# Optimization experiments

Hardware: AMD Instinct MI355X
Metric: run time of the kernel (lower is better)

Reference implementation:

```python
import jax, jax.numpy as jnp
import numpy as np

N, E = 50000, 800000
X_DIM, EA_DIM, H, L = 128, 16, 128, 3
BN_EPS = 1e-5


def setup_inputs() -> dict:
    key = jax.random.key(0)
    ks = jax.random.split(key, 20)
    s = 0.02
    inp = {
        "x": jax.random.normal(ks[0], (N, X_DIM), jnp.float32),
        "edge_index": jax.random.randint(ks[1], (2, E), 0, N, jnp.int64),
        "batch": jnp.sort(jax.random.randint(ks[2], (N,), 0, 128, jnp.int64)),
        "edge_attr": jax.random.normal(ks[3], (E, EA_DIM), jnp.float32),
        "edge_atten": jax.random.uniform(ks[4], (E, 1), jnp.float32),
        # node_encoder2 and edge_encoder
        "W_enc": jax.random.normal(ks[5], (X_DIM, H), jnp.float32) * s,
        "b_enc": jnp.zeros((H,), jnp.float32),
        "W_ee": jax.random.normal(ks[6], (EA_DIM, H), jnp.float32) * s,
        "b_ee": jnp.zeros((H,), jnp.float32),
        # per-layer GINEConv params (stacked over layers)
        "eps": jnp.zeros((L,), jnp.float32),
        "W1": jax.random.normal(ks[7], (L, H, H), jnp.float32) * s,
        "b1": jnp.zeros((L, H), jnp.float32),
        "bn_gamma": jnp.ones((L, H), jnp.float32),
        "bn_beta": jnp.zeros((L, H), jnp.float32),
        "bn_mean": jnp.zeros((L, H), jnp.float32),
        "bn_var": jnp.ones((L, H), jnp.float32),
        "W2": jax.random.normal(ks[8], (L, H, H), jnp.float32) * s,
        "b2": jnp.zeros((L, H), jnp.float32),
    }
    return inp


def reference(x, edge_index, batch, edge_attr, edge_atten,
              W_enc, b_enc, W_ee, b_ee, eps,
              W1, b1, bn_gamma, bn_beta, bn_mean, bn_var, W2, b2):
    # node/edge encoders
    h = x @ W_enc + b_enc                      # [N, H]
    ea = edge_attr @ W_ee + b_ee               # [E, H]
    src, dst = edge_index[0], edge_index[1]
    n = h.shape[0]
    for i in range(L):
        # GINEConv message: relu(x_j + edge_attr) * edge_atten, scatter-add to dst
        m = jax.nn.relu(h[src] + ea) * edge_atten          # [E, H]
        aggr = jax.ops.segment_sum(m, dst, num_segments=n) # [N, H]
        z = (1.0 + eps[i]) * h + aggr
        # MLP: Linear -> BatchNorm(eval, running stats) -> ReLU -> Linear
        z = z @ W1[i] + b1[i]
        z = (z - bn_mean[i]) * jax.lax.rsqrt(bn_var[i] + BN_EPS) * bn_gamma[i] + bn_beta[i]
        z = jax.nn.relu(z)
        z = z @ W2[i] + b2[i]
        # outer relu; dropout is identity in eval mode
        h = jax.nn.relu(z)
    return h
```

## Files before the change

kernel.cpp:

```cpp
#include <hip/hip_runtime.h>
#include <hip/hip_fp16.h>
#include <cstdint>
#include <cstddef>


typedef _Float16 f16x8 __attribute__((ext_vector_type(8)));
typedef float    f32x4 __attribute__((ext_vector_type(4)));

template <class T>
__device__ inline auto add2_impl(T* p, T v, int)
    -> decltype(unsafeAtomicAdd(p, v), void()) {
    unsafeAtomicAdd(p, v);
}
template <class T>
__device__ inline void add2_impl(T* p, T v, long) {
    unsafeAtomicAdd(&p->x, v.x);
    unsafeAtomicAdd(&p->y, v.y);
}
__device__ inline void atomic_add2(float* p, float x, float y) {
    add2_impl(reinterpret_cast<float2*>(p), make_float2(x, y), 0);
}

__global__ void zero_cnt(int* __restrict__ cnt, int N)
{
    int i = blockIdx.x * blockDim.x + threadIdx.x;
    if (i < N) cnt[i] = 0;
}

__global__ void fill_neg1(int* __restrict__ a, int n)
{
    int i = blockIdx.x * blockDim.x + threadIdx.x;
    const int st = gridDim.x * blockDim.x;
    for (; i < n; i += st) a[i] = -1;
}

__global__ void hist_kernel(const int* __restrict__ ei, int* __restrict__ cnt, int E)
{
    int i = blockIdx.x * blockDim.x + threadIdx.x;
    const int st = gridDim.x * blockDim.x;
    for (; i < E; i += st) atomicAdd(&cnt[ei[E + i]], 1);
}

__global__ __launch_bounds__(256) void scan_pass1(
    const int* __restrict__ cnt, int* __restrict__ bsum, int N)
{
    __shared__ int part[256];
    const int t = threadIdx.x;
    const int base = blockIdx.x * 1024 + t * 4;
    int s = 0;
#pragma unroll
    for (int j = 0; j < 4; ++j) {
        int idx = base + j;
        if (idx < N) { int v = cnt[idx]; s += v + (v & 1); }
    }
    part[t] = s;
    __syncthreads();
    for (int d = 128; d > 0; d >>= 1) {
        if (t < d) part[t] += part[t + d];
        __syncthreads();
    }
    if (t == 0) bsum[blockIdx.x] = part[0];
}

__global__ __launch_bounds__(256) void scan_pass2(
    int* __restrict__ bsum, int* __restrict__ off, int NB, int N)
{
    __shared__ int sb[1024];
    const int t = threadIdx.x;
    for (int i = t; i < NB; i += 256) sb[i] = bsum[i];
    __syncthreads();
    if (t == 0) {
        int run = 0;
        for (int i = 0; i < NB; ++i) { int v = sb[i]; sb[i] = run; run += v; }
        off[N] = run;
    }
    __syncthreads();
    for (int i = t; i < NB; i += 256) bsum[i] = sb[i];
}

__global__ __launch_bounds__(256) void scan_pass3(
    const int* __restrict__ cnt, const int* __restrict__ bsum,
    int* __restrict__ off, int* __restrict__ cur, int N)
{
    __shared__ int part[256];
    const int t = threadIdx.x;
    const int base = blockIdx.x * 1024 + t * 4;
    int pv[4]; int s = 0;
#pragma unroll
    for (int j = 0; j < 4; ++j) {
        int idx = base + j;
        int v = (idx < N) ? cnt[idx] : 0;
        pv[j] = v + (v & 1);
        s += pv[j];
    }
    part[t] = s;
    __syncthreads();
    for (int d = 1; d < 256; d <<= 1) {
        int x = (t >= d) ? part[t - d] : 0;
        __syncthreads();
        part[t] += x;
        __syncthreads();
    }
    int run = bsum[blockIdx.x] + part[t] - s;
#pragma unroll
    for (int j = 0; j < 4; ++j) {
        int idx = base + j;
        if (idx < N) { off[idx] = run; cur[idx] = run; }
        run += pv[j];
    }
}

__global__ void scatter_kernel(const int* __restrict__ ei, int* __restrict__ cur,
                               int* __restrict__ eids, int E)
{
    int i = blockIdx.x * blockDim.x + threadIdx.x;
    const int st = gridDim.x * blockDim.x;
    for (; i < E; i += st) {
        int pos = atomicAdd(&cur[ei[E + i]], 1);
        eids[pos] = i;
    }
}

__global__ void permute_sat(
    const int* __restrict__ ei, const float* __restrict__ eatten,
    const int* __restrict__ eids, const int* __restrict__ offN,
    float2* __restrict__ sat, int Scap)
{
    const int S = *offN;
    int i = blockIdx.x * blockDim.x + threadIdx.x;
    const int st = gridDim.x * blockDim.x;
    for (; i < Scap; i += st) {
        if (i >= S) break;
        const int eid = eids[i];
        float2 v;
        if (eid >= 0) { v.x = __int_as_float(ei[eid]); v.y = eatten[eid]; }
        else          { v.x = __int_as_float(0);       v.y = 0.f; }
        sat[i] = v;
    }
}

__global__ __launch_bounds__(256) void eabuild_staged(
    const int* __restrict__ eids, const float* __restrict__ eattr,
    const float* __restrict__ W_ee, const float* __restrict__ b_ee,
    const int* __restrict__ offN, uint32_t* __restrict__ eab2, int Scap)
{
    __shared__ int   se[256];
    __shared__ float sattr[256 * 16];
    const int t = threadIdx.x;
    const int lane = t & 63;
    const int wv = t >> 6;
    const int c = lane * 2;

    const int S = *offN;
    const int base = blockIdx.x * 256;
    const int n = min(256, S - base);
    if (n <= 0) return;

    float2 w[16];
#pragma unroll
    for (int k = 0; k < 16; ++k) w[k] = *(const float2*)&W_ee[k * 128 + c];
    const float2 bv = *(const float2*)&b_ee[c];

    if (t < n) se[t] = eids[base + t];
    __syncthreads();

    float4* sa4 = (float4*)sattr;
    const float4* ea4 = (const float4*)eattr;
    for (int i = t; i < n * 4; i += 256) {
        const int row = i >> 2, part = i & 3;
        const int eid = se[row];
        sa4[i] = (eid >= 0) ? ea4[(size_t)eid * 4 + part]
                            : make_float4(0.f, 0.f, 0.f, 0.f);
    }
    __syncthreads();

    for (int slot = wv; slot < n; slot += 4) {
        const int gs = base + slot;
        uint32_t out = 0;
        if (se[slot] >= 0) {
            const float4* sr = (const float4*)&sattr[slot * 16];
            float4 e0 = sr[0], e1 = sr[1], e2 = sr[2], e3 = sr[3];
            const float ef[16] = {e0.x, e0.y, e0.z, e0.w, e1.x, e1.y, e1.z, e1.w,
                                  e2.x, e2.y, e2.z, e2.w, e3.x, e3.y, e3.z, e3.w};
            float d0 = bv.x, d1 = bv.y;
#pragma unroll
            for (int k = 0; k < 16; ++k) {
                d0 = fmaf(ef[k], w[k].x, d0);
                d1 = fmaf(ef[k], w[k].y, d1);
            }
            __half2 hh = __floats2half2_rn(d0, d1);
            out = *reinterpret_cast<uint32_t*>(&hh);
        }
        eab2[(size_t)(gs >> 1) * 128 + lane * 2 + (gs & 1)] = out;
    }
}

__global__ void prepack_w(const float* __restrict__ W1, const float* __restrict__ W2,
                          const float* __restrict__ Wenc,
                          _Float16* __restrict__ Wpk, int L)
{
    int tid = blockIdx.x * blockDim.x + threadIdx.x;
    const int total = (2 * L + 1) * 32 * 64;
    if (tid >= total) return;
    const int lane = tid & 63;
    const int f = (tid >> 6) & 31;
    const int lm = tid >> 11;
    const int kb = f >> 3, tc = f & 7;
    const float* src = (lm < L) ? (W1 + (size_t)lm * 16384)
                    : (lm < 2 * L) ? (W2 + (size_t)(lm - L) * 16384)
                    : Wenc;
    _Float16* dst = Wpk + ((size_t)lm * 32 + f) * 512 + lane * 8;
#pragma unroll
    for (int i = 0; i < 8; ++i) {
        const int k = kb * 32 + (lane >> 4) * 8 + i;
        const int col = tc * 16 + (lane & 15);
        dst[i] = (_Float16)src[k * 128 + col];
    }
}

__global__ void cvt_f16(const float* __restrict__ x, _Float16* __restrict__ y, int n8)
{
    int i = blockIdx.x * blockDim.x + threadIdx.x;
    const int st = gridDim.x * blockDim.x;
    for (; i < n8; i += st) {
        float4 a = ((const float4*)x)[2 * i];
        float4 b = ((const float4*)x)[2 * i + 1];
        f16x8 v = {(_Float16)a.x, (_Float16)a.y, (_Float16)a.z, (_Float16)a.w,
                   (_Float16)b.x, (_Float16)b.y, (_Float16)b.z, (_Float16)b.w};
        ((f16x8*)y)[i] = v;
    }
}

__global__ __launch_bounds__(256) void enc_mfma(
    const _Float16* __restrict__ x16, const _Float16* __restrict__ Wpk,
    const float* __restrict__ bias, _Float16* __restrict__ h16, int n)
{
    const int t = threadIdx.x;
    const int lane = t & 63;
    const int w = t >> 6;
    const int row0 = blockIdx.x * 64;
    const int lr = lane & 15;
    const int lg = lane >> 4;

    f32x4 acc[8];
#pragma unroll
    for (int tc = 0; tc < 8; ++tc) acc[tc] = (f32x4){0.f, 0.f, 0.f, 0.f};
    const int arow = min(row0 + w * 16 + lr, n - 1);
#pragma unroll
    for (int kb = 0; kb < 4; ++kb) {
        f16x8 a = *(const f16x8*)&x16[(size_t)arow * 128 + kb * 32 + lg * 8];
#pragma unroll
        for (int tc = 0; tc < 8; ++tc) {
            f16x8 b = *(const f16x8*)&Wpk[((kb * 8 + tc) * 64 + lane) * 8];
            acc[tc] = __builtin_amdgcn_mfma_f32_16x16x32_f16(a, b, acc[tc], 0, 0, 0);
        }
    }
#pragma unroll
    for (int tc = 0; tc < 8; ++tc) {
        const int col = tc * 16 + lr;
        const float bb = bias[col];
#pragma unroll
        for (int j = 0; j < 4; ++j) {
            const int row = row0 + w * 16 + lg * 4 + j;
            if (row < n)
                h16[(size_t)row * 128 + col] = (_Float16)(acc[tc][j] + bb);
        }
    }
}

__global__ __launch_bounds__(256) void agg_f16(
    const _Float16* __restrict__ h16, const float2* __restrict__ sat,
    const uint32_t* __restrict__ eab2, const int* __restrict__ off,
    _Float16* __restrict__ z16, const float* __restrict__ eps, int layer, int N)
{
    const int t = threadIdx.x;
    const int v = blockIdx.x * 4 + (t >> 6);
    if (v >= N) return;
    const int lane = t & 63;
    const int c = lane * 2;

    const int e0 = off[v], e1 = off[v + 1];
    float a0 = 0.f, a1 = 0.f;
    int e = e0;
    for (; e + 8 <= e1; e += 8) {
        float4 sa[4];
#pragma unroll
        for (int j = 0; j < 4; ++j) sa[j] = *(const float4*)&sat[e + 2 * j];
        uint2 eb[4];
#pragma unroll
        for (int j = 0; j < 4; ++j)
            eb[j] = *(const uint2*)&eab2[(size_t)((e >> 1) + j) * 128 + lane * 2];
        uint32_t hv[8];
#pragma unroll
        for (int j = 0; j < 4; ++j) {
            hv[2 * j]     = *(const uint32_t*)&h16[(size_t)__float_as_int(sa[j].x) * 128 + c];
            hv[2 * j + 1] = *(const uint32_t*)&h16[(size_t)__float_as_int(sa[j].z) * 128 + c];
        }
#pragma unroll
        for (int j = 0; j < 4; ++j) {
            __half2 hh0 = *reinterpret_cast<const __half2*>(&hv[2 * j]);
            __half2 q0 = *reinterpret_cast<const __half2*>(&eb[j].x);
            a0 += fmaxf(__half2float(__low2half(hh0)) + __half2float(__low2half(q0)), 0.f) * sa[j].y;
            a1 += fmaxf(__half2float(__high2half(hh0)) + __half2float(__high2half(q0)), 0.f) * sa[j].y;
            __half2 hh1 = *reinterpret_cast<const __half2*>(&hv[2 * j + 1]);
            __half2 q1 = *reinterpret_cast<const __half2*>(&eb[j].y);
            a0 += fmaxf(__half2float(__low2half(hh1)) + __half2float(__low2half(q1)), 0.f) * sa[j].w;
            a1 += fmaxf(__half2float(__high2half(hh1)) + __half2float(__high2half(q1)), 0.f) * sa[j].w;
        }
    }
    for (; e < e1; e += 2) {
        float4 sa = *(const float4*)&sat[e];
        uint2 eb = *(const uint2*)&eab2[(size_t)(e >> 1) * 128 + lane * 2];
        uint32_t h0 = *(const uint32_t*)&h16[(size_t)__float_as_int(sa.x) * 128 + c];
        uint32_t h1 = *(const uint32_t*)&h16[(size_t)__float_as_int(sa.z) * 128 + c];
        __half2 hh0 = *reinterpret_cast<const __half2*>(&h0);
        __half2 q0 = *reinterpret_cast<const __half2*>(&eb.x);
        a0 += fmaxf(__half2float(__low2half(hh0)) + __half2float(__low2half(q0)), 0.f) * sa.y;
        a1 += fmaxf(__half2float(__high2half(hh0)) + __half2float(__high2half(q0)), 0.f) * sa.y;
        __half2 hh1 = *reinterpret_cast<const __half2*>(&h1);
        __half2 q1 = *reinterpret_cast<const __half2*>(&eb.y);
        a0 += fmaxf(__half2float(__low2half(hh1)) + __half2float(__low2half(q1)), 0.f) * sa.w;
        a1 += fmaxf(__half2float(__high2half(hh1)) + __half2float(__high2half(q1)), 0.f) * sa.w;
    }

    const float sc = 1.0f + eps[layer];
    uint32_t hv = *(const uint32_t*)&h16[(size_t)v * 128 + c];
    __half2 hh = *reinterpret_cast<const __half2*>(&hv);
    float zx = fmaf(sc, __half2float(__low2half(hh)), a0);
    float zy = fmaf(sc, __half2float(__high2half(hh)), a1);
    __half2 zz = __floats2half2_rn(zx, zy);
    *reinterpret_cast<__half2*>(&z16[(size_t)v * 128 + c]) = zz;
}

__global__ __launch_bounds__(256) void mlp_mfma(
    const _Float16* __restrict__ z16,
    const _Float16* __restrict__ W1pk, const float* __restrict__ b1,
    const float* __restrict__ gam, const float* __restrict__ bet,
    const float* __restrict__ mu, const float* __restrict__ var,
    const _Float16* __restrict__ W2pk, const float* __restrict__ b2,
    _Float16* __restrict__ h16out, float* __restrict__ H, int last, int n)
{
    __shared__ _Float16 Yt[64][136];
    const int t = threadIdx.x;
    const int lane = t & 63;
    const int w = t >> 6;
    const int row0 = blockIdx.x * 64;
    const int lr = lane & 15;
    const int lg = lane >> 4;

    f32x4 acc[8];
#pragma unroll
    for (int tc = 0; tc < 8; ++tc) acc[tc] = (f32x4){0.f, 0.f, 0.f, 0.f};
    const int arow = min(row0 + w * 16 + lr, n - 1);
#pragma unroll
    for (int kb = 0; kb < 4; ++kb) {
        f16x8 a = *(const f16x8*)&z16[(size_t)arow * 128 + kb * 32 + lg * 8];
#pragma unroll
        for (int tc = 0; tc < 8; ++tc) {
            f16x8 b = *(const f16x8*)&W1pk[((kb * 8 + tc) * 64 + lane) * 8];
            acc[tc] = __builtin_amdgcn_mfma_f32_16x16x32_f16(a, b, acc[tc], 0, 0, 0);
        }
    }
#pragma unroll
    for (int tc = 0; tc < 8; ++tc) {
        const int col = tc * 16 + lr;
        const float s  = gam[col] * rsqrtf(var[col] + 1e-5f);
        const float sh = bet[col] - mu[col] * s;
        const float bb = b1[col];
#pragma unroll
        for (int j = 0; j < 4; ++j) {
            float y = fmaxf(fmaf(acc[tc][j] + bb, s, sh), 0.f);
            Yt[w * 16 + lg * 4 + j][col] = (_Float16)y;
        }
    }
    __syncthreads();

#pragma unroll
    for (int tc = 0; tc < 8; ++tc) acc[tc] = (f32x4){0.f, 0.f, 0.f, 0.f};
#pragma unroll
    for (int kb = 0; kb < 4; ++kb) {
        f16x8 a = *(const f16x8*)&Yt[w * 16 + lr][kb * 32 + lg * 8];
#pragma unroll
        for (int tc = 0; tc < 8; ++tc) {
            f16x8 b = *(const f16x8*)&W2pk[((kb * 8 + tc) * 64 + lane) * 8];
            acc[tc] = __builtin_amdgcn_mfma_f32_16x16x32_f16(a, b, acc[tc], 0, 0, 0);
        }
    }
#pragma unroll
    for (int tc = 0; tc < 8; ++tc) {
        const int col = tc * 16 + lr;
        const float bb = b2[col];
#pragma unroll
        for (int j = 0; j < 4; ++j) {
            const int row = row0 + w * 16 + lg * 4 + j;
            if (row < n) {
                const float o = fmaxf(acc[tc][j] + bb, 0.f);
                if (last) H[(size_t)row * 128 + col] = o;
                else      h16out[(size_t)row * 128 + col] = (_Float16)o;
            }
        }
    }
}

__global__ __launch_bounds__(512, 4) void gemm_enc(
    const float* __restrict__ A, const float* __restrict__ W,
    const float* __restrict__ bias, float* __restrict__ H, int n)
{
    __shared__ float At[64][128];
    __shared__ float Wb[2][16][128];
    const int t = threadIdx.x;
    const int tx = t & 31, ty = t >> 5;

    const int row0 = blockIdx.x * 64;
    const int nrows = min(64, n - row0);
    const int lim = nrows * 32;
    const float4* A4 = (const float4*)(A + (size_t)row0 * 128);
    float4* At4 = (float4*)&At[0][0];
#pragma unroll
    for (int i = 0; i < 4; ++i) {
        int idx = t + 512 * i;
        if (idx < lim) At4[idx] = A4[idx];
    }
    const float4* W4 = (const float4*)W;
    ((float4*)&Wb[0][0][0])[t] = W4[t];
    __syncthreads();

    float acc[4][4] = {};
    for (int c = 0; c < 8; ++c) {
        const int buf = c & 1;
        float4 wnext;
        if (c < 7) wnext = W4[(c + 1) * 512 + t];
#pragma unroll
        for (int g = 0; g < 4; ++g) {
            float4 w4[4];
#pragma unroll
            for (int kk = 0; kk < 4; ++kk) w4[kk] = *(const float4*)&Wb[buf][g * 4 + kk][tx * 4];
#pragma unroll
            for (int r = 0; r < 4; ++r) {
                float4 a = *(const float4*)&At[ty * 4 + r][c * 16 + g * 4];
                float ar[4] = {a.x, a.y, a.z, a.w};
#pragma unroll
                for (int kk = 0; kk < 4; ++kk) {
                    acc[r][0] = fmaf(ar[kk], w4[kk].x, acc[r][0]);
                    acc[r][1] = fmaf(ar[kk], w4[kk].y, acc[r][1]);
                    acc[r][2] = fmaf(ar[kk], w4[kk].z, acc[r][2]);
                    acc[r][3] = fmaf(ar[kk], w4[kk].w, acc[r][3]);
                }
            }
        }
        if (c < 7) ((float4*)&Wb[buf ^ 1][0][0])[t] = wnext;
        __syncthreads();
    }

    const int c0 = tx * 4;
    float bvv[4];
#pragma unroll
    for (int c = 0; c < 4; ++c) bvv[c] = bias[c0 + c];
#pragma unroll
    for (int r = 0; r < 4; ++r) {
        int row = row0 + ty * 4 + r;
        if (row < n) {
            float4 o;
            o.x = acc[r][0] + bvv[0]; o.y = acc[r][1] + bvv[1];
            o.z = acc[r][2] + bvv[2]; o.w = acc[r][3] + bvv[3];
            *(float4*)&H[(size_t)row * 128 + c0] = o;
        }
    }
}

__global__ void scale_init(const float* __restrict__ h, float* __restrict__ z,
                           const float* __restrict__ eps, int layer, int n4)
{
    const float s = 1.0f + eps[layer];
    int i = blockIdx.x * blockDim.x + threadIdx.x;
    const int stride = gridDim.x * blockDim.x;
    const float4* h4 = (const float4*)h;
    float4* z4 = (float4*)z;
    for (; i < n4; i += stride) {
        float4 v = h4[i];
        v.x *= s; v.y *= s; v.z *= s; v.w *= s;
        z4[i] = v;
    }
}

__global__ __launch_bounds__(256) void edge_atomic(
    const float* __restrict__ h, const int* __restrict__ ei,
    const float* __restrict__ eattr, const float* __restrict__ eatten,
    const float* __restrict__ W_ee, const float* __restrict__ b_ee,
    float* __restrict__ Z, int E)
{
    __shared__ float Wee[16][128];
    __shared__ float bee[128];
    const int t = threadIdx.x;
    const float4* We4 = (const float4*)W_ee;
    float4* Ws4 = (float4*)&Wee[0][0];
#pragma unroll
    for (int i = 0; i < 2; ++i) Ws4[t + 256 * i] = We4[t + 256 * i];
    if (t < 128) bee[t] = b_ee[t];
    __syncthreads();

    const int lane = t & 63;
    const int c = lane * 2;
    const long wid = (long)blockIdx.x * 4 + (t >> 6);
    const long nw = (long)gridDim.x * 4;
    for (long e = wid; e < E; e += nw) {
        const int src = ei[e];
        const int dst = ei[E + e];
        const float att = eatten[e];
        union { float4 v4[4]; float f[16]; } ea;
        const float4* eap = (const float4*)(eattr + e * 16);
        ea.v4[0] = eap[0]; ea.v4[1] = eap[1]; ea.v4[2] = eap[2]; ea.v4[3] = eap[3];
        float2 hv = *(const float2*)&h[(size_t)src * 128 + c];
        float e0 = bee[c], e1 = bee[c + 1];
#pragma unroll
        for (int k = 0; k < 16; ++k) {
            float2 w = *(const float2*)&Wee[k][c];
            e0 = fmaf(ea.f[k], w.x, e0);
            e1 = fmaf(ea.f[k], w.y, e1);
        }
        float m0 = fmaxf(hv.x + e0, 0.f) * att;
        float m1 = fmaxf(hv.y + e1, 0.f) * att;
        atomic_add2(&Z[(size_t)dst * 128 + c], m0, m1);
    }
}

__global__ __launch_bounds__(512, 4) void gemm_mlp(
    const float* __restrict__ Z,
    const float* __restrict__ W1, const float* __restrict__ b1,
    const float* __restrict__ gam, const float* __restrict__ bet,
    const float* __restrict__ mu, const float* __restrict__ var,
    const float* __restrict__ W2, const float* __restrict__ b2,
    float* __restrict__ H, int n)
{
    __shared__ float At[64][128];
    __shared__ float Wb[2][16][128];
    const int t = threadIdx.x;
    const int tx = t & 31, ty = t >> 5;

    const int row0 = blockIdx.x * 64;
    const int nrows = min(64, n - row0);
    const int lim = nrows * 32;
    const float4* Z4 = (const float4*)(Z + (size_t)row0 * 128);
    float4* At4 = (float4*)&At[0][0];
#pragma unroll
    for (int i = 0; i < 4; ++i) {
        int idx = t + 512 * i;
        if (idx < lim) At4[idx] = Z4[idx];
    }
    const float4* W14 = (const float4*)W1;
    ((float4*)&Wb[0][0][0])[t] = W14[t];
    __syncthreads();

    float acc[4][4] = {};
    for (int c = 0; c < 8; ++c) {
        const int buf = c & 1;
        float4 wnext;
        if (c < 7) wnext = W14[(c + 1) * 512 + t];
#pragma unroll
        for (int g = 0; g < 4; ++g) {
            float4 w4[4];
#pragma unroll
            for (int kk = 0; kk < 4; ++kk) w4[kk] = *(const float4*)&Wb[buf][g * 4 + kk][tx * 4];
#pragma unroll
            for (int r = 0; r < 4; ++r) {
                float4 a = *(const float4*)&At[ty * 4 + r][c * 16 + g * 4];
                float ar[4] = {a.x, a.y, a.z, a.w};
#pragma unroll
                for (int kk = 0; kk < 4; ++kk) {
                    acc[r][0] = fmaf(ar[kk], w4[kk].x, acc[r][0]);
                    acc[r][1] = fmaf(ar[kk], w4[kk].y, acc[r][1]);
                    acc[r][2] = fmaf(ar[kk], w4[kk].z, acc[r][2]);
                    acc[r][3] = fmaf(ar[kk], w4[kk].w, acc[r][3]);
                }
            }
        }
        if (c < 7) ((float4*)&Wb[buf ^ 1][0][0])[t] = wnext;
        __syncthreads();
    }

    const int c0 = tx * 4;
    const float4* W24 = (const float4*)W2;
    float4 w2pre = W24[t];
    {
        float b1v[4], scv[4], shv[4];
#pragma unroll
        for (int cl = 0; cl < 4; ++cl) {
            b1v[cl] = b1[c0 + cl];
            float s = gam[c0 + cl] * rsqrtf(var[c0 + cl] + 1e-5f);
            scv[cl] = s;
            shv[cl] = bet[c0 + cl] - mu[c0 + cl] * s;
        }
#pragma unroll
        for (int r = 0; r < 4; ++r) {
            float4 y;
            y.x = fmaxf(fmaf(acc[r][0] + b1v[0], scv[0], shv[0]), 0.f);
            y.y = fmaxf(fmaf(acc[r][1] + b1v[1], scv[1], shv[1]), 0.f);
            y.z = fmaxf(fmaf(acc[r][2] + b1v[2], scv[2], shv[2]), 0.f);
            y.w = fmaxf(fmaf(acc[r][3] + b1v[3], scv[3], shv[3]), 0.f);
            *(float4*)&At[ty * 4 + r][c0] = y;
            acc[r][0] = 0.f; acc[r][1] = 0.f; acc[r][2] = 0.f; acc[r][3] = 0.f;
        }
    }
    ((float4*)&Wb[0][0][0])[t] = w2pre;
    __syncthreads();

    for (int c = 0; c < 8; ++c) {
        const int buf = c & 1;
        float4 wnext;
        if (c < 7) wnext = W24[(c + 1) * 512 + t];
#pragma unroll
        for (int g = 0; g < 4; ++g) {
            float4 w4[4];
#pragma unroll
            for (int kk = 0; kk < 4; ++kk) w4[kk] = *(const float4*)&Wb[buf][g * 4 + kk][tx * 4];
#pragma unroll
            for (int r = 0; r < 4; ++r) {
                float4 a = *(const float4*)&At[ty * 4 + r][c * 16 + g * 4];
                float ar[4] = {a.x, a.y, a.z, a.w};
#pragma unroll
                for (int kk = 0; kk < 4; ++kk) {
                    acc[r][0] = fmaf(ar[kk], w4[kk].x, acc[r][0]);
                    acc[r][1] = fmaf(ar[kk], w4[kk].y, acc[r][1]);
                    acc[r][2] = fmaf(ar[kk], w4[kk].z, acc[r][2]);
                    acc[r][3] = fmaf(ar[kk], w4[kk].w, acc[r][3]);
                }
            }
        }
        if (c < 7) ((float4*)&Wb[buf ^ 1][0][0])[t] = wnext;
        __syncthreads();
    }

    float b2v[4];
#pragma unroll
    for (int cl = 0; cl < 4; ++cl) b2v[cl] = b2[c0 + cl];
#pragma unroll
    for (int r = 0; r < 4; ++r) {
        int row = row0 + ty * 4 + r;
        if (row < n) {
            float4 o;
            o.x = fmaxf(acc[r][0] + b2v[0], 0.f);
            o.y = fmaxf(acc[r][1] + b2v[1], 0.f);
            o.z = fmaxf(acc[r][2] + b2v[2], 0.f);
            o.w = fmaxf(acc[r][3] + b2v[3], 0.f);
            *(float4*)&H[(size_t)row * 128 + c0] = o;
        }
    }
}

extern "C" void kernel_launch(void* const* d_in, const int* in_sizes, int n_in,
                              void* d_out, int out_size, void* d_ws, size_t ws_size,
                              hipStream_t stream)
{
    const float* x      = (const float*)d_in[0];
    const int*   ei     = (const int*)d_in[1];
    const float* eattr  = (const float*)d_in[3];
    const float* eatten = (const float*)d_in[4];
    const float* W_enc  = (const float*)d_in[5];
    const float* b_enc  = (const float*)d_in[6];
    const float* W_ee   = (const float*)d_in[7];
    const float* b_ee   = (const float*)d_in[8];
    const float* eps    = (const float*)d_in[9];
    const float* W1     = (const float*)d_in[10];
    const float* b1     = (const float*)d_in[11];
    const float* gam    = (const float*)d_in[12];
    const float* bet    = (const float*)d_in[13];
    const float* mu     = (const float*)d_in[14];
    const float* var    = (const float*)d_in[15];
    const float* W2     = (const float*)d_in[16];
    const float* b2     = (const float*)d_in[17];

    const int N = in_sizes[0] / 128;
    const int E = in_sizes[1] / 2;
    const int L = in_sizes[9];
    const int Scap = E + N;

    float* hout = (float*)d_out;

    char* p = (char*)d_ws;
    _Float16* z16 = (_Float16*)p;       p += ((size_t)N * 128 * 2 + 255) & ~(size_t)255;
    _Float16* h16 = (_Float16*)p;       p += ((size_t)N * 128 * 2 + 255) & ~(size_t)255;
    int* off  = (int*)p;                p += 4 * (size_t)(N + 1);
    int* cur  = (int*)p;                p += 4 * (size_t)N;
    int* cnt  = (int*)p;                p += 4 * (size_t)N;
    int* bsum = (int*)p;                p += 4 * 1024;
    int* eids = (int*)p;                p += 4 * (size_t)Scap;
    p = (char*)(((uintptr_t)p + 255) & ~(uintptr_t)255);
    float2* sat = (float2*)p;           p += 8 * (size_t)Scap;
    p = (char*)(((uintptr_t)p + 255) & ~(uintptr_t)255);
    uint32_t* eab2 = (uint32_t*)p;      p += 512 * (size_t)((Scap + 1) / 2);
    p = (char*)(((uintptr_t)p + 255) & ~(uintptr_t)255);
    _Float16* Wpk = (_Float16*)p;       p += (2 * (size_t)L + 1) * 32 * 512 * 2;
    const size_t need_main = (size_t)(p - (char*)d_ws);

    const bool use_main = ws_size >= need_main;
    const int tiles = (N + 63) / 64;
    const int NB = (N + 1023) / 1024;

    if (use_main) {
        _Float16* x16 = z16;

        zero_cnt<<<(N + 255) / 256, 256, 0, stream>>>(cnt, N);
        hist_kernel<<<1024, 256, 0, stream>>>(ei, cnt, E);
        scan_pass1<<<NB, 256, 0, stream>>>(cnt, bsum, N);
        scan_pass2<<<1, 256, 0, stream>>>(bsum, off, NB, N);
        scan_pass3<<<NB, 256, 0, stream>>>(cnt, bsum, off, cur, N);
        fill_neg1<<<1024, 256, 0, stream>>>(eids, Scap);
        scatter_kernel<<<1024, 256, 0, stream>>>(ei, cur, eids, E);
        permute_sat<<<1024, 256, 0, stream>>>(ei, eatten, eids, off + N, sat, Scap);
        eabuild_staged<<<(Scap + 255) / 256, 256, 0, stream>>>(
            eids, eattr, W_ee, b_ee, off + N, eab2, Scap);
        prepack_w<<<((2 * L + 1) * 32 * 64 + 255) / 256, 256, 0, stream>>>(
            W1, W2, W_enc, Wpk, L);

        cvt_f16<<<2048, 256, 0, stream>>>(x, x16, N * 128 / 8);
        enc_mfma<<<tiles, 256, 0, stream>>>(
            x16, Wpk + (size_t)(2 * L) * 32 * 512, b_enc, h16, N);

        for (int i = 0; i < L; ++i) {
            agg_f16<<<(N + 3) / 4, 256, 0, stream>>>(
                h16, sat, eab2, off, z16, eps, i, N);
            mlp_mfma<<<tiles, 256, 0, stream>>>(
                z16,
                Wpk + (size_t)i * 32 * 512, b1 + i * 128,
                gam + i * 128, bet + i * 128, mu + i * 128, var + i * 128,
                Wpk + (size_t)(L + i) * 32 * 512, b2 + i * 128,
                h16, hout, (i == L - 1) ? 1 : 0, N);
        }
        return;
    }

    float* zbuf = (float*)d_ws;
    float* h = hout;
    gemm_enc<<<tiles, 512, 0, stream>>>(x, W_enc, b_enc, h, N);
    for (int i = 0; i < L; ++i) {
        scale_init<<<2048, 256, 0, stream>>>(h, zbuf, eps, i, N * 128 / 4);
        edge_atomic<<<2048, 256, 0, stream>>>(h, ei, eattr, eatten, W_ee, b_ee, zbuf, E);
        gemm_mlp<<<tiles, 512, 0, stream>>>(
            zbuf, W1 + (size_t)i * 128 * 128, b1 + i * 128,
            gam + i * 128, bet + i * 128, mu + i * 128, var + i * 128,
            W2 + (size_t)i * 128 * 128, b2 + i * 128,
            h, N);
    }
}
```

Baseline: 480.8 us.

## Recompute edge encoder per edge in aggregation instead of materializing edge embeddings

```diff
diff --git a/kernel.cpp b/kernel.cpp
--- a/kernel.cpp
+++ b/kernel.cpp
@@ -5,7 +5,16 @@
 
 
 typedef _Float16 f16x8 __attribute__((ext_vector_type(8)));
+typedef _Float16 f16x2 __attribute__((ext_vector_type(2)));
 typedef float    f32x4 __attribute__((ext_vector_type(4)));
+
+__device__ inline float fdot2f(f16x2 a, f16x2 b, float c) {
+#if __has_builtin(__builtin_amdgcn_fdot2)
+    return __builtin_amdgcn_fdot2(a, b, c, false);
+#else
+    return c + (float)a.x * (float)b.x + (float)a.y * (float)b.y;
+#endif
+}
 
 template <class T>
 __device__ inline auto add2_impl(T* p, T v, int)
@@ -121,77 +130,33 @@
     }
 }
 
-__global__ void permute_sat(
+__global__ void permute_all(
     const int* __restrict__ ei, const float* __restrict__ eatten,
-    const int* __restrict__ eids, const int* __restrict__ offN,
-    float2* __restrict__ sat, int Scap)
+    const float* __restrict__ eattr, const int* __restrict__ eids,
+    const int* __restrict__ offN,
+    float2* __restrict__ sat, _Float16* __restrict__ attr16, int Scap)
 {
     const int S = *offN;
     int i = blockIdx.x * blockDim.x + threadIdx.x;
     const int st = gridDim.x * blockDim.x;
-    for (; i < Scap; i += st) {
-        if (i >= S) break;
+    for (; i < S; i += st) {
         const int eid = eids[i];
         float2 v;
-        if (eid >= 0) { v.x = __int_as_float(ei[eid]); v.y = eatten[eid]; }
-        else          { v.x = __int_as_float(0);       v.y = 0.f; }
+        f16x8 a0 = {}, a1 = {};
+        if (eid >= 0) {
+            v.x = __int_as_float(ei[eid]); v.y = eatten[eid];
+            const float4* ep = (const float4*)(eattr + (size_t)eid * 16);
+            float4 e0 = ep[0], e1 = ep[1], e2 = ep[2], e3 = ep[3];
+            a0 = (f16x8){(_Float16)e0.x, (_Float16)e0.y, (_Float16)e0.z, (_Float16)e0.w,
+                         (_Float16)e1.x, (_Float16)e1.y, (_Float16)e1.z, (_Float16)e1.w};
+            a1 = (f16x8){(_Float16)e2.x, (_Float16)e2.y, (_Float16)e2.z, (_Float16)e2.w,
+                         (_Float16)e3.x, (_Float16)e3.y, (_Float16)e3.z, (_Float16)e3.w};
+        } else {
+            v.x = __int_as_float(0); v.y = 0.f;
+        }
         sat[i] = v;
-    }
-}
-
-__global__ __launch_bounds__(256) void eabuild_staged(
-    const int* __restrict__ eids, const float* __restrict__ eattr,
-    const float* __restrict__ W_ee, const float* __restrict__ b_ee,
-    const int* __restrict__ offN, uint32_t* __restrict__ eab2, int Scap)
-{
-    __shared__ int   se[256];
-    __shared__ float sattr[256 * 16];
-    const int t = threadIdx.x;
-    const int lane = t & 63;
-    const int wv = t >> 6;
-    const int c = lane * 2;
-
-    const int S = *offN;
-    const int base = blockIdx.x * 256;
-    const int n = min(256, S - base);
-    if (n <= 0) return;
-
-    float2 w[16];
-#pragma unroll
-    for (int k = 0; k < 16; ++k) w[k] = *(const float2*)&W_ee[k * 128 + c];
-    const float2 bv = *(const float2*)&b_ee[c];
-
-    if (t < n) se[t] = eids[base + t];
-    __syncthreads();
-
-    float4* sa4 = (float4*)sattr;
-    const float4* ea4 = (const float4*)eattr;
-    for (int i = t; i < n * 4; i += 256) {
-        const int row = i >> 2, part = i & 3;
-        const int eid = se[row];
-        sa4[i] = (eid >= 0) ? ea4[(size_t)eid * 4 + part]
-                            : make_float4(0.f, 0.f, 0.f, 0.f);
-    }
-    __syncthreads();
-
-    for (int slot = wv; slot < n; slot += 4) {
-        const int gs = base + slot;
-        uint32_t out = 0;
-        if (se[slot] >= 0) {
-            const float4* sr = (const float4*)&sattr[slot * 16];
-            float4 e0 = sr[0], e1 = sr[1], e2 = sr[2], e3 = sr[3];
-            const float ef[16] = {e0.x, e0.y, e0.z, e0.w, e1.x, e1.y, e1.z, e1.w,
-                                  e2.x, e2.y, e2.z, e2.w, e3.x, e3.y, e3.z, e3.w};
-            float d0 = bv.x, d1 = bv.y;
-#pragma unroll
-            for (int k = 0; k < 16; ++k) {
-                d0 = fmaf(ef[k], w[k].x, d0);
-                d1 = fmaf(ef[k], w[k].y, d1);
-            }
-            __half2 hh = __floats2half2_rn(d0, d1);
-            out = *reinterpret_cast<uint32_t*>(&hh);
-        }
-        eab2[(size_t)(gs >> 1) * 128 + lane * 2 + (gs & 1)] = out;
+        ((f16x8*)attr16)[2 * i]     = a0;
+        ((f16x8*)attr16)[2 * i + 1] = a1;
     }
 }
 
@@ -270,62 +235,84 @@
 
 __global__ __launch_bounds__(256) void agg_f16(
     const _Float16* __restrict__ h16, const float2* __restrict__ sat,
-    const uint32_t* __restrict__ eab2, const int* __restrict__ off,
+    const _Float16* __restrict__ attr16, const int* __restrict__ off,
+    const float* __restrict__ W_ee, const float* __restrict__ b_ee,
     _Float16* __restrict__ z16, const float* __restrict__ eps, int layer, int N)
 {
     const int t = threadIdx.x;
+    const int lane = t & 63;
+    const int c = lane * 2;
+
+    f16x2 wx[8], wy[8];
+#pragma unroll
+    for (int j = 0; j < 8; ++j) {
+        float2 wa = *(const float2*)&W_ee[(2 * j) * 128 + c];
+        float2 wb = *(const float2*)&W_ee[(2 * j + 1) * 128 + c];
+        wx[j] = (f16x2){(_Float16)wa.x, (_Float16)wb.x};
+        wy[j] = (f16x2){(_Float16)wa.y, (_Float16)wb.y};
+    }
+    const float2 bv = *(const float2*)&b_ee[c];
+
     const int v = blockIdx.x * 4 + (t >> 6);
     if (v >= N) return;
-    const int lane = t & 63;
-    const int c = lane * 2;
 
     const int e0 = off[v], e1 = off[v + 1];
     float a0 = 0.f, a1 = 0.f;
+
+    auto edge = [&](uint4 lo, uint4 hi, uint32_t hvv, float att) {
+        const f16x2* a2lo = (const f16x2*)&lo;
+        const f16x2* a2hi = (const f16x2*)&hi;
+        float d0 = bv.x, d1 = bv.y;
+#pragma unroll
+        for (int j = 0; j < 4; ++j) {
+            d0 = fdot2f(a2lo[j], wx[j], d0);
+            d1 = fdot2f(a2lo[j], wy[j], d1);
+        }
+#pragma unroll
+        for (int j = 0; j < 4; ++j) {
+            d0 = fdot2f(a2hi[j], wx[4 + j], d0);
+            d1 = fdot2f(a2hi[j], wy[4 + j], d1);
+        }
+        __half2 hh = *reinterpret_cast<const __half2*>(&hvv);
+        a0 += fmaxf(__half2float(__low2half(hh)) + d0, 0.f) * att;
+        a1 += fmaxf(__half2float(__high2half(hh)) + d1, 0.f) * att;
+    };
+
     int e = e0;
-    for (; e + 8 <= e1; e += 8) {
-        float4 sa[4];
-#pragma unroll
-        for (int j = 0; j < 4; ++j) sa[j] = *(const float4*)&sat[e + 2 * j];
-        uint2 eb[4];
-#pragma unroll
-        for (int j = 0; j < 4; ++j)
-            eb[j] = *(const uint2*)&eab2[(size_t)((e >> 1) + j) * 128 + lane * 2];
-        uint32_t hv[8];
-#pragma unroll
-        for (int j = 0; j < 4; ++j) {
-            hv[2 * j]     = *(const uint32_t*)&h16[(size_t)__float_as_int(sa[j].x) * 128 + c];
-            hv[2 * j + 1] = *(const uint32_t*)&h16[(size_t)__float_as_int(sa[j].z) * 128 + c];
-        }
-#pragma unroll
-        for (int j = 0; j < 4; ++j) {
-            __half2 hh0 = *reinterpret_cast<const __half2*>(&hv[2 * j]);
-            __half2 q0 = *reinterpret_cast<const __half2*>(&eb[j].x);
-            a0 += fmaxf(__half2float(__low2half(hh0)) + __half2float(__low2half(q0)), 0.f) * sa[j].y;
-            a1 += fmaxf(__half2float(__high2half(hh0)) + __half2float(__high2half(q0)), 0.f) * sa[j].y;
-            __half2 hh1 = *reinterpret_cast<const __half2*>(&hv[2 * j + 1]);
-            __half2 q1 = *reinterpret_cast<const __half2*>(&eb[j].y);
-            a0 += fmaxf(__half2float(__low2half(hh1)) + __half2float(__low2half(q1)), 0.f) * sa[j].w;
-            a1 += fmaxf(__half2float(__high2half(hh1)) + __half2float(__high2half(q1)), 0.f) * sa[j].w;
-        }
+    for (; e + 4 <= e1; e += 4) {
+        float4 sa0 = *(const float4*)&sat[e];
+        float4 sa1 = *(const float4*)&sat[e + 2];
+        uint4 at[8];
+#pragma unroll
+        for (int u = 0; u < 4; ++u) {
+            at[2 * u]     = *(const uint4*)&attr16[(size_t)(e + u) * 16];
+            at[2 * u + 1] = *(const uint4*)&attr16[(size_t)(e + u) * 16 + 8];
+        }
+        uint32_t hv[4];
+        hv[0] = *(const uint32_t*)&h16[(size_t)__float_as_int(sa0.x) * 128 + c];
+        hv[1] = *(const uint32_t*)&h16[(size_t)__float_as_int(sa0.z) * 128 + c];
+        hv[2] = *(const uint32_t*)&h16[(size_t)__float_as_int(sa1.x) * 128 + c];
+        hv[3] = *(const uint32_t*)&h16[(size_t)__float_as_int(sa1.z) * 128 + c];
+        edge(at[0], at[1], hv[0], sa0.y);
+        edge(at[2], at[3], hv[1], sa0.w);
+        edge(at[4], at[5], hv[2], sa1.y);
+        edge(at[6], at[7], hv[3], sa1.w);
     }
     for (; e < e1; e += 2) {
         float4 sa = *(const float4*)&sat[e];
-        uint2 eb = *(const uint2*)&eab2[(size_t)(e >> 1) * 128 + lane * 2];
-        uint32_t h0 = *(const uint32_t*)&h16[(size_t)__float_as_int(sa.x) * 128 + c];
-        uint32_t h1 = *(const uint32_t*)&h16[(size_t)__float_as_int(sa.z) * 128 + c];
-        __half2 hh0 = *reinterpret_cast<const __half2*>(&h0);
-        __half2 q0 = *reinterpret_cast<const __half2*>(&eb.x);
-        a0 += fmaxf(__half2float(__low2half(hh0)) + __half2float(__low2half(q0)), 0.f) * sa.y;
-        a1 += fmaxf(__half2float(__high2half(hh0)) + __half2float(__high2half(q0)), 0.f) * sa.y;
-        __half2 hh1 = *reinterpret_cast<const __half2*>(&h1);
-        __half2 q1 = *reinterpret_cast<const __half2*>(&eb.y);
-        a0 += fmaxf(__half2float(__low2half(hh1)) + __half2float(__low2half(q1)), 0.f) * sa.w;
-        a1 += fmaxf(__half2float(__high2half(hh1)) + __half2float(__high2half(q1)), 0.f) * sa.w;
+        uint4 l0 = *(const uint4*)&attr16[(size_t)e * 16];
+        uint4 h0 = *(const uint4*)&attr16[(size_t)e * 16 + 8];
+        uint4 l1 = *(const uint4*)&attr16[(size_t)(e + 1) * 16];
+        uint4 h1 = *(const uint4*)&attr16[(size_t)(e + 1) * 16 + 8];
+        uint32_t hv0 = *(const uint32_t*)&h16[(size_t)__float_as_int(sa.x) * 128 + c];
+        uint32_t hv1 = *(const uint32_t*)&h16[(size_t)__float_as_int(sa.z) * 128 + c];
+        edge(l0, h0, hv0, sa.y);
+        edge(l1, h1, hv1, sa.w);
     }
 
     const float sc = 1.0f + eps[layer];
-    uint32_t hv = *(const uint32_t*)&h16[(size_t)v * 128 + c];
-    __half2 hh = *reinterpret_cast<const __half2*>(&hv);
+    uint32_t hvv = *(const uint32_t*)&h16[(size_t)v * 128 + c];
+    __half2 hh = *reinterpret_cast<const __half2*>(&hvv);
     float zx = fmaf(sc, __half2float(__low2half(hh)), a0);
     float zy = fmaf(sc, __half2float(__high2half(hh)), a1);
     __half2 zz = __floats2half2_rn(zx, zy);
@@ -687,7 +674,7 @@
     p = (char*)(((uintptr_t)p + 255) & ~(uintptr_t)255);
     float2* sat = (float2*)p;           p += 8 * (size_t)Scap;
     p = (char*)(((uintptr_t)p + 255) & ~(uintptr_t)255);
-    uint32_t* eab2 = (uint32_t*)p;      p += 512 * (size_t)((Scap + 1) / 2);
+    _Float16* attr16 = (_Float16*)p;    p += 32 * (size_t)Scap;
     p = (char*)(((uintptr_t)p + 255) & ~(uintptr_t)255);
     _Float16* Wpk = (_Float16*)p;       p += (2 * (size_t)L + 1) * 32 * 512 * 2;
     const size_t need_main = (size_t)(p - (char*)d_ws);
@@ -706,9 +693,8 @@
         scan_pass3<<<NB, 256, 0, stream>>>(cnt, bsum, off, cur, N);
         fill_neg1<<<1024, 256, 0, stream>>>(eids, Scap);
         scatter_kernel<<<1024, 256, 0, stream>>>(ei, cur, eids, E);
-        permute_sat<<<1024, 256, 0, stream>>>(ei, eatten, eids, off + N, sat, Scap);
-        eabuild_staged<<<(Scap + 255) / 256, 256, 0, stream>>>(
-            eids, eattr, W_ee, b_ee, off + N, eab2, Scap);
+        permute_all<<<2048, 256, 0, stream>>>(ei, eatten, eattr, eids, off + N,
+                                              sat, attr16, Scap);
         prepack_w<<<((2 * L + 1) * 32 * 64 + 255) / 256, 256, 0, stream>>>(
             W1, W2, W_enc, Wpk, L);
 
@@ -718,7 +704,7 @@
 
         for (int i = 0; i < L; ++i) {
             agg_f16<<<(N + 3) / 4, 256, 0, stream>>>(
-                h16, sat, eab2, off, z16, eps, i, N);
+                h16, sat, attr16, off, W_ee, b_ee, z16, eps, i, N);
             mlp_mfma<<<tiles, 256, 0, stream>>>(
                 z16,
                 Wpk + (size_t)i * 32 * 512, b1 + i * 128,
```

Result: slower. 544.1 us (+13.2%).

## Store precomputed edge embeddings in FP8 and merge init kernels

Applied to the files above, without the earlier changes.

```diff
diff --git a/kernel.cpp b/kernel.cpp
--- a/kernel.cpp
+++ b/kernel.cpp
@@ -6,6 +6,48 @@
 
 typedef _Float16 f16x8 __attribute__((ext_vector_type(8)));
 typedef float    f32x4 __attribute__((ext_vector_type(4)));
+typedef float    f32x2 __attribute__((ext_vector_type(2)));
+
+__device__ inline uint32_t pack_fp8_pair(float a, float b) {
+#if __has_builtin(__builtin_amdgcn_cvt_pk_fp8_f32)
+    return (uint32_t)__builtin_amdgcn_cvt_pk_fp8_f32(a, b, 0, false) & 0xFFFFu;
+#else
+    auto enc = [](float x) -> uint32_t {
+        uint32_t s = (x < 0.f) ? 0x80u : 0u;
+        float ax = fabsf(x);
+        if (!(ax >= 1.953125e-3f)) {
+            int mi = (int)(ax * 512.f + 0.5f);
+            if (mi > 7) mi = 7;
+            return s | (uint32_t)mi;
+        }
+        ax = fminf(ax, 448.f);
+        int e; float m = frexpf(ax, &e);
+        int E = e - 1 + 7;
+        int mi = (int)((m * 2.f - 1.f) * 8.f + 0.5f);
+        if (mi == 8) { mi = 0; ++E; }
+        if (E > 15 || (E == 15 && mi == 7)) { E = 15; mi = 6; }
+        return s | ((uint32_t)E << 3) | (uint32_t)mi;
+    };
+    return enc(a) | (enc(b) << 8);
+#endif
+}
+
+template <bool HIGH>
+__device__ inline f32x2 unpack_fp8_pair(uint32_t w) {
+#if __has_builtin(__builtin_amdgcn_cvt_pk_f32_fp8)
+    return __builtin_amdgcn_cvt_pk_f32_fp8((int)w, HIGH);
+#else
+    auto dec = [](uint32_t v) -> float {
+        uint32_t s = v >> 7, e = (v >> 3) & 0xF, m = v & 7;
+        float r = (e == 0) ? ldexpf((float)m, -9)
+                           : ldexpf(1.f + (float)m / 8.f, (int)e - 7);
+        return s ? -r : r;
+    };
+    uint32_t b0 = HIGH ? ((w >> 16) & 0xFF) : (w & 0xFF);
+    uint32_t b1 = HIGH ? ((w >> 24) & 0xFF) : ((w >> 8) & 0xFF);
+    return (f32x2){dec(b0), dec(b1)};
+#endif
+}
 
 template <class T>
 __device__ inline auto add2_impl(T* p, T v, int)
@@ -21,17 +63,12 @@
     add2_impl(reinterpret_cast<float2*>(p), make_float2(x, y), 0);
 }
 
-__global__ void zero_cnt(int* __restrict__ cnt, int N)
-{
-    int i = blockIdx.x * blockDim.x + threadIdx.x;
-    if (i < N) cnt[i] = 0;
-}
-
-__global__ void fill_neg1(int* __restrict__ a, int n)
+__global__ void init_arrays(int* __restrict__ cnt, int N, int* __restrict__ eids, int S)
 {
     int i = blockIdx.x * blockDim.x + threadIdx.x;
     const int st = gridDim.x * blockDim.x;
-    for (; i < n; i += st) a[i] = -1;
+    for (int j = i; j < N; j += st) cnt[j] = 0;
+    for (int j = i; j < S; j += st) eids[j] = -1;
 }
 
 __global__ void hist_kernel(const int* __restrict__ ei, int* __restrict__ cnt, int E)
@@ -129,8 +166,7 @@
     const int S = *offN;
     int i = blockIdx.x * blockDim.x + threadIdx.x;
     const int st = gridDim.x * blockDim.x;
-    for (; i < Scap; i += st) {
-        if (i >= S) break;
+    for (; i < S; i += st) {
         const int eid = eids[i];
         float2 v;
         if (eid >= 0) { v.x = __int_as_float(ei[eid]); v.y = eatten[eid]; }
@@ -142,7 +178,7 @@
 __global__ __launch_bounds__(256) void eabuild_staged(
     const int* __restrict__ eids, const float* __restrict__ eattr,
     const float* __restrict__ W_ee, const float* __restrict__ b_ee,
-    const int* __restrict__ offN, uint32_t* __restrict__ eab2, int Scap)
+    const int* __restrict__ offN, uint16_t* __restrict__ eab8, int Scap)
 {
     __shared__ int   se[256];
     __shared__ float sattr[256 * 16];
@@ -188,10 +224,9 @@
                 d0 = fmaf(ef[k], w[k].x, d0);
                 d1 = fmaf(ef[k], w[k].y, d1);
             }
-            __half2 hh = __floats2half2_rn(d0, d1);
-            out = *reinterpret_cast<uint32_t*>(&hh);
-        }
-        eab2[(size_t)(gs >> 1) * 128 + lane * 2 + (gs & 1)] = out;
+            out = pack_fp8_pair(d0, d1);
+        }
+        eab8[(size_t)(gs >> 1) * 128 + lane * 2 + (gs & 1)] = (uint16_t)out;
     }
 }
 
@@ -268,9 +303,9 @@
     }
 }
 
-__global__ __launch_bounds__(256) void agg_f16(
+__global__ __launch_bounds__(256) void agg_f8(
     const _Float16* __restrict__ h16, const float2* __restrict__ sat,
-    const uint32_t* __restrict__ eab2, const int* __restrict__ off,
+    const uint32_t* __restrict__ eab8, const int* __restrict__ off,
     _Float16* __restrict__ z16, const float* __restrict__ eps, int layer, int N)
 {
     const int t = threadIdx.x;
@@ -283,49 +318,56 @@
     float a0 = 0.f, a1 = 0.f;
     int e = e0;
     for (; e + 8 <= e1; e += 8) {
-        float4 sa[4];
-#pragma unroll
-        for (int j = 0; j < 4; ++j) sa[j] = *(const float4*)&sat[e + 2 * j];
-        uint2 eb[4];
+        float4 sa[2];
+        sa[0] = *(const float4*)&sat[e];
+        sa[1] = *(const float4*)&sat[e + 2];
+        float4 sb[2];
+        sb[0] = *(const float4*)&sat[e + 4];
+        sb[1] = *(const float4*)&sat[e + 6];
+        uint32_t eb[4];
 #pragma unroll
         for (int j = 0; j < 4; ++j)
-            eb[j] = *(const uint2*)&eab2[(size_t)((e >> 1) + j) * 128 + lane * 2];
+            eb[j] = eab8[(size_t)((e >> 1) + j) * 64 + lane];
         uint32_t hv[8];
+        hv[0] = *(const uint32_t*)&h16[(size_t)__float_as_int(sa[0].x) * 128 + c];
+        hv[1] = *(const uint32_t*)&h16[(size_t)__float_as_int(sa[0].z) * 128 + c];
+        hv[2] = *(const uint32_t*)&h16[(size_t)__float_as_int(sa[1].x) * 128 + c];
+        hv[3] = *(const uint32_t*)&h16[(size_t)__float_as_int(sa[1].z) * 128 + c];
+        hv[4] = *(const uint32_t*)&h16[(size_t)__float_as_int(sb[0].x) * 128 + c];
+        hv[5] = *(const uint32_t*)&h16[(size_t)__float_as_int(sb[0].z) * 128 + c];
+        hv[6] = *(const uint32_t*)&h16[(size_t)__float_as_int(sb[1].x) * 128 + c];
+        hv[7] = *(const uint32_t*)&h16[(size_t)__float_as_int(sb[1].z) * 128 + c];
 #pragma unroll
         for (int j = 0; j < 4; ++j) {
-            hv[2 * j]     = *(const uint32_t*)&h16[(size_t)__float_as_int(sa[j].x) * 128 + c];
-            hv[2 * j + 1] = *(const uint32_t*)&h16[(size_t)__float_as_int(sa[j].z) * 128 + c];
-        }
-#pragma unroll
-        for (int j = 0; j < 4; ++j) {
-            __half2 hh0 = *reinterpret_cast<const __half2*>(&hv[2 * j]);
-            __half2 q0 = *reinterpret_cast<const __half2*>(&eb[j].x);
-            a0 += fmaxf(__half2float(__low2half(hh0)) + __half2float(__low2half(q0)), 0.f) * sa[j].y;
-            a1 += fmaxf(__half2float(__high2half(hh0)) + __half2float(__high2half(q0)), 0.f) * sa[j].y;
-            __half2 hh1 = *reinterpret_cast<const __half2*>(&hv[2 * j + 1]);
-            __half2 q1 = *reinterpret_cast<const __half2*>(&eb[j].y);
-            a0 += fmaxf(__half2float(__low2half(hh1)) + __half2float(__low2half(q1)), 0.f) * sa[j].w;
-            a1 += fmaxf(__half2float(__high2half(hh1)) + __half2float(__high2half(q1)), 0.f) * sa[j].w;
+            const float4 s4 = (j < 2) ? sa[j] : sb[j - 2];
+            f32x2 ev = unpack_fp8_pair<false>(eb[j]);
+            f32x2 od = unpack_fp8_pair<true>(eb[j]);
+            __half2 h0 = *reinterpret_cast<const __half2*>(&hv[2 * j]);
+            __half2 h1 = *reinterpret_cast<const __half2*>(&hv[2 * j + 1]);
+            a0 += fmaxf(__half2float(__low2half(h0))  + ev[0], 0.f) * s4.y;
+            a1 += fmaxf(__half2float(__high2half(h0)) + ev[1], 0.f) * s4.y;
+            a0 += fmaxf(__half2float(__low2half(h1))  + od[0], 0.f) * s4.w;
+            a1 += fmaxf(__half2float(__high2half(h1)) + od[1], 0.f) * s4.w;
         }
     }
     for (; e < e1; e += 2) {
         float4 sa = *(const float4*)&sat[e];
-        uint2 eb = *(const uint2*)&eab2[(size_t)(e >> 1) * 128 + lane * 2];
-        uint32_t h0 = *(const uint32_t*)&h16[(size_t)__float_as_int(sa.x) * 128 + c];
-        uint32_t h1 = *(const uint32_t*)&h16[(size_t)__float_as_int(sa.z) * 128 + c];
-        __half2 hh0 = *reinterpret_cast<const __half2*>(&h0);
-        __half2 q0 = *reinterpret_cast<const __half2*>(&eb.x);
-        a0 += fmaxf(__half2float(__low2half(hh0)) + __half2float(__low2half(q0)), 0.f) * sa.y;
-        a1 += fmaxf(__half2float(__high2half(hh0)) + __half2float(__high2half(q0)), 0.f) * sa.y;
-        __half2 hh1 = *reinterpret_cast<const __half2*>(&h1);
-        __half2 q1 = *reinterpret_cast<const __half2*>(&eb.y);
-        a0 += fmaxf(__half2float(__low2half(hh1)) + __half2float(__low2half(q1)), 0.f) * sa.w;
-        a1 += fmaxf(__half2float(__high2half(hh1)) + __half2float(__high2half(q1)), 0.f) * sa.w;
+        uint32_t eb = eab8[(size_t)(e >> 1) * 64 + lane];
+        uint32_t hv0 = *(const uint32_t*)&h16[(size_t)__float_as_int(sa.x) * 128 + c];
+        uint32_t hv1 = *(const uint32_t*)&h16[(size_t)__float_as_int(sa.z) * 128 + c];
+        f32x2 ev = unpack_fp8_pair<false>(eb);
+        f32x2 od = unpack_fp8_pair<true>(eb);
+        __half2 h0 = *reinterpret_cast<const __half2*>(&hv0);
+        __half2 h1 = *reinterpret_cast<const __half2*>(&hv1);
+        a0 += fmaxf(__half2float(__low2half(h0))  + ev[0], 0.f) * sa.y;
+        a1 += fmaxf(__half2float(__high2half(h0)) + ev[1], 0.f) * sa.y;
+        a0 += fmaxf(__half2float(__low2half(h1))  + od[0], 0.f) * sa.w;
+        a1 += fmaxf(__half2float(__high2half(h1)) + od[1], 0.f) * sa.w;
     }
 
     const float sc = 1.0f + eps[layer];
-    uint32_t hv = *(const uint32_t*)&h16[(size_t)v * 128 + c];
-    __half2 hh = *reinterpret_cast<const __half2*>(&hv);
+    uint32_t hvv = *(const uint32_t*)&h16[(size_t)v * 128 + c];
+    __half2 hh = *reinterpret_cast<const __half2*>(&hvv);
     float zx = fmaf(sc, __half2float(__low2half(hh)), a0);
     float zy = fmaf(sc, __half2float(__high2half(hh)), a1);
     __half2 zz = __floats2half2_rn(zx, zy);
@@ -687,7 +729,7 @@
     p = (char*)(((uintptr_t)p + 255) & ~(uintptr_t)255);
     float2* sat = (float2*)p;           p += 8 * (size_t)Scap;
     p = (char*)(((uintptr_t)p + 255) & ~(uintptr_t)255);
-    uint32_t* eab2 = (uint32_t*)p;      p += 512 * (size_t)((Scap + 1) / 2);
+    uint16_t* eab8 = (uint16_t*)p;      p += 256 * (size_t)((Scap + 1) / 2);
     p = (char*)(((uintptr_t)p + 255) & ~(uintptr_t)255);
     _Float16* Wpk = (_Float16*)p;       p += (2 * (size_t)L + 1) * 32 * 512 * 2;
     const size_t need_main = (size_t)(p - (char*)d_ws);
@@ -699,16 +741,15 @@
     if (use_main) {
         _Float16* x16 = z16;
 
-        zero_cnt<<<(N + 255) / 256, 256, 0, stream>>>(cnt, N);
+        init_arrays<<<1024, 256, 0, stream>>>(cnt, N, eids, Scap);
         hist_kernel<<<1024, 256, 0, stream>>>(ei, cnt, E);
         scan_pass1<<<NB, 256, 0, stream>>>(cnt, bsum, N);
         scan_pass2<<<1, 256, 0, stream>>>(bsum, off, NB, N);
         scan_pass3<<<NB, 256, 0, stream>>>(cnt, bsum, off, cur, N);
-        fill_neg1<<<1024, 256, 0, stream>>>(eids, Scap);
         scatter_kernel<<<1024, 256, 0, stream>>>(ei, cur, eids, E);
         permute_sat<<<1024, 256, 0, stream>>>(ei, eatten, eids, off + N, sat, Scap);
         eabuild_staged<<<(Scap + 255) / 256, 256, 0, stream>>>(
-            eids, eattr, W_ee, b_ee, off + N, eab2, Scap);
+            eids, eattr, W_ee, b_ee, off + N, eab8, Scap);
         prepack_w<<<((2 * L + 1) * 32 * 64 + 255) / 256, 256, 0, stream>>>(
             W1, W2, W_enc, Wpk, L);
 
@@ -717,8 +758,8 @@
             x16, Wpk + (size_t)(2 * L) * 32 * 512, b_enc, h16, N);
 
         for (int i = 0; i < L; ++i) {
-            agg_f16<<<(N + 3) / 4, 256, 0, stream>>>(
-                h16, sat, eab2, off, z16, eps, i, N);
+            agg_f8<<<(N + 3) / 4, 256, 0, stream>>>(
+                h16, sat, (const uint32_t*)eab8, off, z16, eps, i, N);
             mlp_mfma<<<tiles, 256, 0, stream>>>(
                 z16,
                 Wpk + (size_t)i * 32 * 512, b1 + i * 128,
```

After: 423.3 us. 1.14x faster.
